# Performance work log

Hardware: AMD Instinct MI355X
Metric: run time of the kernel (lower is better)

Reference implementation:

```python
import jax, jax.numpy as jnp
import numpy as np

B, C, H, W = 8, 16, 128, 128
P = H * W            # pixel_number = 16384
KN = 16              # kernel_number_per_pixel
CK = C * 9           # in_channel * kernel_size = 144


def setup_inputs() -> dict:
    key = jax.random.key(0)
    k1, k2, k3 = jax.random.split(key, 3)
    x = jax.random.normal(k1, (B, C, H, W), dtype=jnp.float32)
    weights = jax.random.normal(k2, (P, KN, CK), dtype=jnp.float32)
    hash_idx = jax.random.randint(k3, (P, CK), 0, C * H * W, dtype=jnp.int64)
    return {"x": x, "weights": weights, "hash_idx": hash_idx}


def reference(x, weights, hash_idx):
    b, c, h, w = x.shape
    img_size = c * h * w
    flat = x.reshape(-1)  # [B*C*H*W]
    # per-batch offset of the per-pixel hash table (torch fallback branch)
    idx = hash_idx[None, :, :] + (jnp.arange(b, dtype=hash_idx.dtype) * img_size)[:, None, None]  # [B,P,CK]
    patches = flat[idx]  # [B, P, CK] hash-indexed gather (im2col)
    # weights [P,KN,CK] @ patches [P,CK,B] -> [P,KN,B]; transpose(0,2) -> [B,KN,P]
    return jnp.einsum('pkc,bpc->bkp', weights, patches)
```

## Files before the change

kernel.cpp:

```cpp
#include <hip/hip_runtime.h>
#include <hip/hip_bf16.h>

#define P_TOTAL 16384
#define KN      16
#define CK      144
#define BATCH   8
#define IMG     262144
#define NP      8
#define NCHUNK  (P_TOTAL / NP)


__device__ __forceinline__ float blo16(uint32_t u) {
    union { uint32_t i; float f; } v; v.i = u << 16;        return v.f;
}
__device__ __forceinline__ float bhi16(uint32_t u) {
    union { uint32_t i; float f; } v; v.i = u & 0xffff0000u; return v.f;
}

__global__ __launch_bounds__(256) void transpose_x_bf16(
    const float* __restrict__ x, float4* __restrict__ xt)
{
    const int i = blockIdx.x * 256 + threadIdx.x;
    union { __hip_bfloat16 h[8]; float4 f4; } u;
#pragma unroll
    for (int b = 0; b < BATCH; ++b)
        u.h[b] = __float2bfloat16(
            __builtin_nontemporal_load(&x[(size_t)b * IMG + i]));
    xt[i] = u.f4;
}

__global__ __launch_bounds__(256) void abc2d_xt_bf16lds(
    const float4* __restrict__ xt,
    const float*  __restrict__ w,
    const int*    __restrict__ hidx,
    float* __restrict__ out)
{
    __shared__ float4 patchv[2][CK];
    __shared__ float  outbuf[KN * BATCH * NP];

    const int bid   = blockIdx.x;
    const int chunk = (bid & 7) * (NCHUNK / 8) + (bid >> 3);
    const int p0    = chunk * NP;
    const int t     = threadIdx.x;
    const int k     = t >> 4;
    const int cs    = t & 15;
    const bool do_g = (t < CK);

    float wcur[9], wnxt[9];
    float4 g;
    int id_nxt = 0;

    {
        const float* wp = w + (size_t)p0 * (KN * CK) + (size_t)k * CK + cs;
#pragma unroll
        for (int i = 0; i < 9; ++i)
            wcur[i] = __builtin_nontemporal_load(wp + 16 * i);
    }
    if (do_g) {
        const int id0 = hidx[p0 * CK + t];
        g = xt[id0];
        id_nxt = hidx[(p0 + 1) * CK + t];
    }

#pragma unroll
    for (int j = 0; j < NP; ++j) {
        const int jb = j & 1;

        if (j + 1 < NP) {
            const float* wp = w + (size_t)(p0 + j + 1) * (KN * CK) + (size_t)k * CK + cs;
#pragma unroll
            for (int i = 0; i < 9; ++i)
                wnxt[i] = __builtin_nontemporal_load(wp + 16 * i);
        }

        if (do_g) patchv[jb][t] = g;
        __syncthreads();

        if (do_g && j + 1 < NP) {
            g = xt[id_nxt];
            if (j + 2 < NP) id_nxt = hidx[(p0 + j + 2) * CK + t];
        }

        float acc[BATCH];
#pragma unroll
        for (int b = 0; b < BATCH; ++b) acc[b] = 0.f;

#pragma unroll
        for (int i = 0; i < 9; ++i) {
            const int c = cs + 16 * i;
            const float wv = wcur[i];
            const float4 q = patchv[jb][c];
            const uint32_t d0 = __float_as_uint(q.x);
            const uint32_t d1 = __float_as_uint(q.y);
            const uint32_t d2 = __float_as_uint(q.z);
            const uint32_t d3 = __float_as_uint(q.w);
            acc[0] += wv * blo16(d0);
            acc[1] += wv * bhi16(d0);
            acc[2] += wv * blo16(d1);
            acc[3] += wv * bhi16(d1);
            acc[4] += wv * blo16(d2);
            acc[5] += wv * bhi16(d2);
            acc[6] += wv * blo16(d3);
            acc[7] += wv * bhi16(d3);
        }

#pragma unroll
        for (int b = 0; b < BATCH; ++b) {
            float v = acc[b];
            v += __shfl_xor(v, 1);
            v += __shfl_xor(v, 2);
            v += __shfl_xor(v, 4);
            v += __shfl_xor(v, 8);
            acc[b] = v;
        }

        if (cs == 0) {
#pragma unroll
            for (int b = 0; b < BATCH; ++b)
                outbuf[(k * BATCH + b) * NP + j] = acc[b];
        }

        if (j + 1 < NP) {
#pragma unroll
            for (int i = 0; i < 9; ++i) wcur[i] = wnxt[i];
        }
    }

    __syncthreads();
    if (t < KN * BATCH) {
        const int kk = t >> 3;
        const int bb = t & 7;
        const float* src = &outbuf[(kk * BATCH + bb) * NP];
        const float4 v0 = *reinterpret_cast<const float4*>(src);
        const float4 v1 = *reinterpret_cast<const float4*>(src + 4);
        float* dst = &out[((size_t)bb * KN + kk) * P_TOTAL + p0];
        *reinterpret_cast<float4*>(dst)     = v0;
        *reinterpret_cast<float4*>(dst + 4) = v1;
    }
}

#define PSTRIDE 12
__global__ __launch_bounds__(256) void abc2d_direct(
    const float* __restrict__ x, const float* __restrict__ w,
    const int* __restrict__ hidx, float* __restrict__ out)
{
    __shared__ float patch[CK * PSTRIDE];
    const int bid = blockIdx.x;
    const int p   = (bid & 7) * (P_TOTAL / 8) + (bid >> 3);
    const int t   = threadIdx.x;
    const int k   = t >> 4;
    const int cs  = t & 15;

    if (t < CK) {
        const int id = hidx[p * CK + t];
        float v[BATCH];
#pragma unroll
        for (int b = 0; b < BATCH; ++b) v[b] = x[(size_t)b * IMG + (size_t)id];
        float* pr = &patch[t * PSTRIDE];
        *reinterpret_cast<float4*>(pr)     = make_float4(v[0], v[1], v[2], v[3]);
        *reinterpret_cast<float4*>(pr + 4) = make_float4(v[4], v[5], v[6], v[7]);
    }

    const float* wp = w + (size_t)p * (KN * CK) + (size_t)k * CK;
    float wreg[9];
#pragma unroll
    for (int i = 0; i < 9; ++i) wreg[i] = wp[cs + 16 * i];
    __syncthreads();

    float acc[BATCH];
#pragma unroll
    for (int b = 0; b < BATCH; ++b) acc[b] = 0.f;
#pragma unroll
    for (int i = 0; i < 9; ++i) {
        const float wv = wreg[i];
        const float* pr = &patch[(cs + 16 * i) * PSTRIDE];
        const float4 q0 = *reinterpret_cast<const float4*>(pr);
        const float4 q1 = *reinterpret_cast<const float4*>(pr + 4);
        acc[0] += wv * q0.x; acc[1] += wv * q0.y; acc[2] += wv * q0.z; acc[3] += wv * q0.w;
        acc[4] += wv * q1.x; acc[5] += wv * q1.y; acc[6] += wv * q1.z; acc[7] += wv * q1.w;
    }
#pragma unroll
    for (int b = 0; b < BATCH; ++b) {
        float v = acc[b];
        v += __shfl_xor(v, 1); v += __shfl_xor(v, 2);
        v += __shfl_xor(v, 4); v += __shfl_xor(v, 8);
        acc[b] = v;
    }
    if (cs == 0) {
#pragma unroll
        for (int b = 0; b < BATCH; ++b)
            out[(size_t)b * (KN * P_TOTAL) + (size_t)k * P_TOTAL + p] = acc[b];
    }
}

extern "C" void kernel_launch(void* const* d_in, const int* in_sizes, int n_in,
                              void* d_out, int out_size, void* d_ws, size_t ws_size,
                              hipStream_t stream) {
    const float* x    = (const float*)d_in[0];
    const float* wts  = (const float*)d_in[1];
    const int*   hidx = (const int*)d_in[2];
    float* out = (float*)d_out;

    const size_t xt_bytes = (size_t)IMG * BATCH * sizeof(__hip_bfloat16);
    if (ws_size >= xt_bytes) {
        float4* xt = (float4*)d_ws;
        transpose_x_bf16<<<IMG / 256, 256, 0, stream>>>(x, xt);
        abc2d_xt_bf16lds<<<NCHUNK, 256, 0, stream>>>(xt, wts, hidx, out);
    } else {
        abc2d_direct<<<P_TOTAL, 256, 0, stream>>>(x, wts, hidx, out);
    }
}
```

Baseline: 235.6 us.

## Gather all chunk patches up front and deepen weight prefetch to two pixels

All hash-indexed gathers for the 8 pixels in a chunk are now issued in one burst into a larger LDS buffer, with a single barrier replacing the per-pixel double-buffered gather and sync. Weight loads are prefetched two pixels ahead instead of one. The aim is to expose more memory-level parallelism for the random gathers and to remove the barriers inside the loop. The cost is more LDS (about 18KB) and more registers, which may reduce occupancy.

```diff
diff --git a/kernel.cpp b/kernel.cpp
--- a/kernel.cpp
+++ b/kernel.cpp
@@ -8,6 +8,7 @@
 #define IMG     262144
 #define NP      8
 #define NCHUNK  (P_TOTAL / NP)
+#define ROWS    (CK * NP)
 
 
 __device__ __forceinline__ float blo16(uint32_t u) {
@@ -29,13 +30,13 @@
     xt[i] = u.f4;
 }
 
-__global__ __launch_bounds__(256) void abc2d_xt_bf16lds(
+__global__ __launch_bounds__(256) void abc2d_xt_burst(
     const float4* __restrict__ xt,
     const float*  __restrict__ w,
     const int*    __restrict__ hidx,
     float* __restrict__ out)
 {
-    __shared__ float4 patchv[2][CK];
+    __shared__ float4 patchv[ROWS];
     __shared__ float  outbuf[KN * BATCH * NP];
 
     const int bid   = blockIdx.x;
@@ -44,52 +45,51 @@
     const int t     = threadIdx.x;
     const int k     = t >> 4;
     const int cs    = t & 15;
-    const bool do_g = (t < CK);
-
-    float wcur[9], wnxt[9];
-    float4 g;
-    int id_nxt = 0;
-
+
+    float wcur[9], wnxt[9], wnx2[9];
     {
-        const float* wp = w + (size_t)p0 * (KN * CK) + (size_t)k * CK + cs;
+        const float* wp0 = w + (size_t)p0 * (KN * CK) + (size_t)k * CK + cs;
 #pragma unroll
         for (int i = 0; i < 9; ++i)
-            wcur[i] = __builtin_nontemporal_load(wp + 16 * i);
-    }
-    if (do_g) {
-        const int id0 = hidx[p0 * CK + t];
-        g = xt[id0];
-        id_nxt = hidx[(p0 + 1) * CK + t];
-    }
+            wcur[i] = __builtin_nontemporal_load(wp0 + 16 * i);
+        const float* wp1 = wp0 + KN * CK;
+#pragma unroll
+        for (int i = 0; i < 9; ++i)
+            wnxt[i] = __builtin_nontemporal_load(wp1 + 16 * i);
+    }
+
+    {
+        const int* hp = hidx + (size_t)p0 * CK;
+        int ids[4];
+#pragma unroll
+        for (int u = 0; u < 4; ++u) ids[u] = hp[t + 256 * u];
+        int id4 = 0;
+        const bool has5 = (t < ROWS - 1024);
+        if (has5) id4 = hp[t + 1024];
+#pragma unroll
+        for (int u = 0; u < 4; ++u) patchv[t + 256 * u] = xt[ids[u]];
+        if (has5) patchv[t + 1024] = xt[id4];
+    }
+    __syncthreads();
 
 #pragma unroll
     for (int j = 0; j < NP; ++j) {
-        const int jb = j & 1;
-
-        if (j + 1 < NP) {
-            const float* wp = w + (size_t)(p0 + j + 1) * (KN * CK) + (size_t)k * CK + cs;
+        if (j + 2 < NP) {
+            const float* wp = w + (size_t)(p0 + j + 2) * (KN * CK) + (size_t)k * CK + cs;
 #pragma unroll
             for (int i = 0; i < 9; ++i)
-                wnxt[i] = __builtin_nontemporal_load(wp + 16 * i);
-        }
-
-        if (do_g) patchv[jb][t] = g;
-        __syncthreads();
-
-        if (do_g && j + 1 < NP) {
-            g = xt[id_nxt];
-            if (j + 2 < NP) id_nxt = hidx[(p0 + j + 2) * CK + t];
+                wnx2[i] = __builtin_nontemporal_load(wp + 16 * i);
         }
 
         float acc[BATCH];
 #pragma unroll
         for (int b = 0; b < BATCH; ++b) acc[b] = 0.f;
 
+        const float4* pj = &patchv[j * CK];
 #pragma unroll
         for (int i = 0; i < 9; ++i) {
-            const int c = cs + 16 * i;
             const float wv = wcur[i];
-            const float4 q = patchv[jb][c];
+            const float4 q = pj[cs + 16 * i];
             const uint32_t d0 = __float_as_uint(q.x);
             const uint32_t d1 = __float_as_uint(q.y);
             const uint32_t d2 = __float_as_uint(q.z);
@@ -120,10 +120,8 @@
                 outbuf[(k * BATCH + b) * NP + j] = acc[b];
         }
 
-        if (j + 1 < NP) {
-#pragma unroll
-            for (int i = 0; i < 9; ++i) wcur[i] = wnxt[i];
-        }
+#pragma unroll
+        for (int i = 0; i < 9; ++i) { wcur[i] = wnxt[i]; wnxt[i] = wnx2[i]; }
     }
 
     __syncthreads();
@@ -205,7 +203,7 @@
     if (ws_size >= xt_bytes) {
         float4* xt = (float4*)d_ws;
         transpose_x_bf16<<<IMG / 256, 256, 0, stream>>>(x, xt);
-        abc2d_xt_bf16lds<<<NCHUNK, 256, 0, stream>>>(xt, wts, hidx, out);
+        abc2d_xt_burst<<<NCHUNK, 256, 0, stream>>>(xt, wts, hidx, out);
     } else {
         abc2d_direct<<<P_TOTAL, 256, 0, stream>>>(x, wts, hidx, out);
     }
```

After: 240.0 us. No clear change (+1.9%).
